# Performance work log

Measured on AMD Instinct MI355X. Metric: run time of the kernel, lower is better.

Reference implementation:

```python
import jax, jax.numpy as jnp
import numpy as np
import math

B, L, D = 4, 4096, 1024
PI = math.pi
LN_EPS = 1e-5


def setup_inputs() -> dict:
    key = jax.random.key(0)
    ks = jax.random.split(key, 16)
    s = 1.0 / math.sqrt(D)
    inp = {
        "x": jax.random.normal(ks[0], (B, L, D), dtype=jnp.float32),
        # Linear weights stored as [in, out] (torch W.T)
        "Wk": jax.random.normal(ks[1], (D, D), dtype=jnp.float32) * s,
        "bk": jnp.zeros((D,), dtype=jnp.float32),
        "Wq": jax.random.normal(ks[2], (D, D), dtype=jnp.float32) * s,
        "bq": jnp.zeros((D,), dtype=jnp.float32),
        "Wv": jax.random.normal(ks[3], (D, D), dtype=jnp.float32) * s,
        "bv": jnp.zeros((D,), dtype=jnp.float32),
        "ln_g": jnp.ones((D,), dtype=jnp.float32),
        "ln_b": jnp.zeros((D,), dtype=jnp.float32),
        "Wo": jax.random.normal(ks[4], (D, D), dtype=jnp.float32) * s,
        "bo": jnp.zeros((D,), dtype=jnp.float32),
        "Wg1": jax.random.normal(ks[5], (D, D // 4), dtype=jnp.float32) * s,
        "bg1": jnp.zeros((D // 4,), dtype=jnp.float32),
        "Wg2": jax.random.normal(ks[6], (D // 4, 1), dtype=jnp.float32) * (2.0 / math.sqrt(D)),
        "bg2": jnp.zeros((1,), dtype=jnp.float32),
        "pos_phases": jax.random.normal(ks[7], (L, D), dtype=jnp.float32) * PI,
    }
    return inp


def _layernorm(x, g, b):
    mu = jnp.mean(x, axis=-1, keepdims=True)
    var = jnp.var(x, axis=-1, keepdims=True)
    return (x - mu) * jax.lax.rsqrt(var + LN_EPS) * g + b


def reference(x, Wk, bk, Wq, bq, Wv, bv, ln_g, ln_b, Wo, bo, Wg1, bg1, Wg2, bg2, pos_phases):
    # dropout is identity in eval mode
    key_phases = jnp.tanh(x @ Wk + bk) * PI          # [B,L,D]
    query_phases = jnp.tanh(x @ Wq + bq) * PI        # [B,L,D]
    V = x @ Wv + bv                                   # [B,L,D]

    cos_k, sin_k = jnp.cos(key_phases), jnp.sin(key_phases)
    cos_q, sin_q = jnp.cos(query_phases), jnp.sin(query_phases)

    mem_real = jnp.cumsum(V * cos_k, axis=1)
    mem_imag = jnp.cumsum(V * sin_k, axis=1)
    content_retrieved = mem_real * cos_q + mem_imag * sin_q

    pp = pos_phases[: x.shape[1]]                     # [L,D]
    cos_p, sin_p = jnp.cos(pp), jnp.sin(pp)
    pos_mem_real = jnp.cumsum(V * cos_p, axis=1)
    pos_mem_imag = jnp.cumsum(V * sin_p, axis=1)
    pos_retrieved = pos_mem_real * cos_p + pos_mem_imag * sin_p

    gate = jax.nn.sigmoid(jax.nn.gelu(x @ Wg1 + bg1) @ Wg2 + bg2)  # [B,L,1]
    combined = gate * content_retrieved + (1.0 - gate) * pos_retrieved

    positions = jnp.arange(1, x.shape[1] + 1, dtype=jnp.float32)
    norm = jnp.sqrt(positions)[None, :, None]
    out = _layernorm(combined / norm, ln_g, ln_b) @ Wo + bo
    return x + out
```

## Files before the change

### kernel.cpp

```cpp
#include <hip/hip_runtime.h>
#include <math.h>

#define B_ 4
#define L_ 4096
#define D_ 1024
#define DG_ 256
#define NC_ 128
#define CL_ 32
#define PI_F 3.14159265358979323846f
#define LN_EPS_F 1e-5f

typedef __attribute__((ext_vector_type(8))) _Float16 f16x8;
typedef __attribute__((ext_vector_type(8))) short s16x8;
typedef __attribute__((ext_vector_type(4))) short s16x4;
typedef __attribute__((ext_vector_type(4))) float f32x4;

__device__ inline short f2h(float f) { return __builtin_bit_cast(short, (_Float16)f); }
__device__ inline float h2f(short s) { return (float)__builtin_bit_cast(_Float16, s); }

__device__ inline float ftanh(float x) {
    float e = __expf(2.0f * x);
    return 1.0f - 2.0f / (e + 1.0f);
}
__device__ inline void fsincos(float x, float* s, float* c) {
    *s = __sinf(x); *c = __cosf(x);
}

__device__ inline void gld16(const void* g, void* l) {
    __builtin_amdgcn_global_load_lds(
        (const __attribute__((address_space(1))) unsigned int*)g,
        (__attribute__((address_space(3))) unsigned int*)l, 16, 0, 0);
}

__global__ __launch_bounds__(256)
void conv_x(const float* __restrict__ x, short* __restrict__ xh, int n8)
{
    int t = blockIdx.x * 256 + threadIdx.x;
    if (t >= n8) return;
    const float4* p = (const float4*)x + (size_t)t * 2;
    float4 a = p[0], b = p[1];
    s16x8 v;
    v[0] = f2h(a.x); v[1] = f2h(a.y); v[2] = f2h(a.z); v[3] = f2h(a.w);
    v[4] = f2h(b.x); v[5] = f2h(b.y); v[6] = f2h(b.z); v[7] = f2h(b.w);
    *(s16x8*)(xh + (size_t)t * 8) = v;
}

__global__ __launch_bounds__(256)
void convT(const float* __restrict__ W, short* __restrict__ Th, int N)
{
    __shared__ float tile[64][65];
    const int n0 = blockIdx.x * 64, k0 = blockIdx.y * 64;
    const int t = threadIdx.x;
    const int r = t >> 4, c4 = (t & 15) * 4;

    #pragma unroll
    for (int i = 0; i < 4; ++i) {
        float4 v = *(const float4*)&W[(size_t)(k0 + r + i * 16) * N + n0 + c4];
        tile[r + i * 16][c4 + 0] = v.x;
        tile[r + i * 16][c4 + 1] = v.y;
        tile[r + i * 16][c4 + 2] = v.z;
        tile[r + i * 16][c4 + 3] = v.w;
    }
    __syncthreads();
    #pragma unroll
    for (int i = 0; i < 4; ++i) {
        const int n = r + i * 16;
        s16x4 o;
        o[0] = f2h(tile[c4 + 0][n]);
        o[1] = f2h(tile[c4 + 1][n]);
        o[2] = f2h(tile[c4 + 2][n]);
        o[3] = f2h(tile[c4 + 3][n]);
        *(s16x4*)&Th[(size_t)(n0 + n) * 1024 + k0 + c4] = o;
    }
}

#define BARRIER() __builtin_amdgcn_s_barrier()
#define PRIO1() __builtin_amdgcn_s_setprio(1)
#define PRIO0() __builtin_amdgcn_s_setprio(0)
#define LGKM0() do { asm volatile("s_waitcnt lgkmcnt(0)" ::: "memory"); \
                     __builtin_amdgcn_sched_barrier(0); } while (0)
#define VMC(N) asm volatile("s_waitcnt vmcnt(" #N ")" ::: "memory")

#define DSR(dst, areg, OFS)                                              \
    asm volatile("ds_read_b128 %0, %1 offset:" OFS                       \
                 : "=v"(dst) : "v"(areg))

#define RDA4(areg)                                                       \
    DSR(af[0], areg, "0");    DSR(af[1], areg, "2048");                  \
    DSR(af[2], areg, "4096"); DSR(af[3], areg, "6144");
#define RDA4H(areg)                                                      \
    DSR(af[0], areg, "8192");  DSR(af[1], areg, "10240");                \
    DSR(af[2], areg, "12288"); DSR(af[3], areg, "14336");
#define RDB4(areg, KK)                                                   \
    DSR(bq[0][KK], areg, "0");    DSR(bq[1][KK], areg, "2048");          \
    DSR(bq[2][KK], areg, "4096"); DSR(bq[3][KK], areg, "6144");

#define MF(MG, KK)                                                       \
    _Pragma("unroll") for (int i_ = 0; i_ < 4; ++i_)                     \
    _Pragma("unroll") for (int n_ = 0; n_ < 4; ++n_)                     \
        acc[(MG)*4 + i_][n_] = __builtin_amdgcn_mfma_f32_16x16x32_f16(   \
            af[i_], bq[n_][KK], acc[(MG)*4 + i_][n_], 0, 0, 0);

template<int EPI, typename OT>
__global__ __launch_bounds__(512, 2)
void mgemm256(const short* __restrict__ A, const short* __restrict__ Bt,
              const float* __restrict__ X, OT* __restrict__ out0,
              short* __restrict__ out1, short* __restrict__ out2,
              const float* __restrict__ b0, const float* __restrict__ b1,
              const float* __restrict__ b2, int M, int N, int K)
{
    extern __shared__ char lds[];

    const int tid = threadIdx.x;
    const int w = tid >> 6, l = tid & 63;
    const int wr = w >> 2, wc = w & 3;
    const int fr = l & 15, kb = l >> 4;
    const int bm = blockIdx.x * 256, bn = blockIdx.y * 256;
    const int np = K >> 7;

    const int s = fr & 7;
    const int cK0 = (((s >> 2) & 1) << 6) | (((kb ^ s) & 3) << 4);
    const int aA0 = (wr << 14) + fr * 128 + cK0;
    const int aA1 = aA0 ^ 64;
    const int aB0 = 32768 + ((wc >> 1) << 14) + ((wc & 1) * 64 + fr) * 128 + cK0;
    const int aB1 = aB0 ^ 64;
    const int aA0o = aA0 + 65536, aA1o = aA1 + 65536;
    const int aB0o = aB0 + 65536, aB1o = aB1 + 65536;

    const int p0 = tid * 16;
    const int sr = p0 >> 7;
    const int sc = (p0 & 127) ^ ((sr & 7) << 4);
    const short* gA = A  + (size_t)(bm + sr) * K + (sc >> 1);
    const short* gB = Bt + (size_t)(bn + sr) * K + (sc >> 1);
    char* ldst = lds + (w << 10);
    const size_t q1 = (size_t)64 * K, q2 = 2 * q1, q3 = 3 * q1;

    f32x4 acc[8][4] = {};
    f16x8 af[4];
    f16x8 bq[4][2];

    gld16(gA,      ldst);          gld16(gA + q1, ldst + 8192);
    gld16(gA + q2, ldst + 16384);  gld16(gA + q3, ldst + 24576);
    gld16(gB,      ldst + 32768);  gld16(gB + q1, ldst + 40960);
    gld16(gB + q2, ldst + 49152);  gld16(gB + q3, ldst + 57344);
    gld16(gA +      64, ldst + 65536);
    gld16(gA + q2 + 64, ldst + 65536 + 16384);
    VMC(2);
    BARRIER();

    const short* gAn = gA + 64;
    const short* gBn = gB + 64;

    for (int pp = 0; pp < np; ++pp) {
        const bool nl = (pp + 1 < np);

        RDA4(aA0); RDB4(aB0, 0);
        gld16(gBn,      ldst + 98304);
        gld16(gBn + q1, ldst + 98304 + 8192);
        BARRIER();
        LGKM0();
        PRIO1(); MF(0, 0); PRIO0();
        BARRIER();

        RDA4(aA1); RDB4(aB1, 1);
        gld16(gBn + q2, ldst + 98304 + 16384);
        gld16(gBn + q3, ldst + 98304 + 24576);
        BARRIER();
        LGKM0();
        PRIO1(); MF(0, 1); PRIO0();
        BARRIER();

        RDA4H(aA0);
        gld16(gAn + q1, ldst + 65536 + 8192);
        gld16(gAn + q3, ldst + 65536 + 24576);
        BARRIER();
        LGKM0();
        PRIO1(); MF(1, 0); PRIO0();
        BARRIER();

        RDA4H(aA1);
        if (nl) { gld16(gAn + 64, ldst); gld16(gAn + 64 + q2, ldst + 16384); }
        BARRIER();
        LGKM0();
        PRIO1(); MF(1, 1); PRIO0();
        VMC(2);
        BARRIER();

        RDA4(aA0o); RDB4(aB0o, 0);
        if (nl) {
            gld16(gBn +      64, ldst + 32768);
            gld16(gBn + q1 + 64, ldst + 40960);
        }
        BARRIER();
        LGKM0();
        PRIO1(); MF(0, 0); PRIO0();
        BARRIER();

        RDA4(aA1o); RDB4(aB1o, 1);
        if (nl) {
            gld16(gBn + q2 + 64, ldst + 49152);
            gld16(gBn + q3 + 64, ldst + 57344);
        }
        BARRIER();
        LGKM0();
        PRIO1(); MF(0, 1); PRIO0();
        BARRIER();

        if (!nl) VMC(0);
        RDA4H(aA0o);
        if (nl) {
            gld16(gAn + q1 + 64, ldst + 8192);
            gld16(gAn + q3 + 64, ldst + 24576);
        }
        BARRIER();
        LGKM0();
        PRIO1(); MF(1, 0); PRIO0();
        BARRIER();

        RDA4H(aA1o);
        if (nl) { gld16(gAn + 128, ldst + 65536); gld16(gAn + 128 + q2, ldst + 65536 + 16384); }
        BARRIER();
        LGKM0();
        PRIO1(); MF(1, 1); PRIO0();
        if (nl) {
            VMC(2);
            BARRIER();
        }
        gAn += 128; gBn += 128;
    }

    if constexpr (EPI == 4) {
        short* op; const float* bp; bool dt;
        if (bn < 1024)      { op = (short*)out0; bp = b0; dt = true;  }
        else if (bn < 2048) { op = out1;         bp = b1; dt = true;  }
        else                { op = out2;         bp = b2; dt = false; }
        const int cb = bn & 1023;
        float bc[4];
        #pragma unroll
        for (int nf = 0; nf < 4; ++nf) bc[nf] = bp[cb + wc * 64 + nf * 16 + fr];
        #pragma unroll
        for (int mf = 0; mf < 8; ++mf)
            #pragma unroll
            for (int rr = 0; rr < 4; ++rr) {
                const int row = bm + wr * 128 + mf * 16 + kb * 4 + rr;
                #pragma unroll
                for (int nf = 0; nf < 4; ++nf) {
                    const int cc = cb + wc * 64 + nf * 16 + fr;
                    float c = acc[mf][nf][rr] + bc[nf];
                    if (dt) c = ftanh(c) * PI_F;
                    op[(size_t)row * 1024 + cc] = f2h(c);
                }
            }
    } else {
        float bc[4];
        #pragma unroll
        for (int nf = 0; nf < 4; ++nf) bc[nf] = b0[bn + wc * 64 + nf * 16 + fr];
        #pragma unroll
        for (int mf = 0; mf < 8; ++mf)
            #pragma unroll
            for (int rr = 0; rr < 4; ++rr) {
                const int row = bm + wr * 128 + mf * 16 + kb * 4 + rr;
                #pragma unroll
                for (int nf = 0; nf < 4; ++nf) {
                    const int col = bn + wc * 64 + nf * 16 + fr;
                    float c = acc[mf][nf][rr] + bc[nf] + X[(size_t)row * N + col];
                    ((float*)out0)[(size_t)row * N + col] = c;
                }
            }
    }
}

#define RDAF(areg)                                                       \
    DSR(af[0], areg, "0");    DSR(af[1], areg, "2048");                  \
    DSR(af[2], areg, "4096"); DSR(af[3], areg, "6144");
#define RDBF(areg)                                                       \
    DSR(bqs[0], areg, "0");    DSR(bqs[1], areg, "2048");                \
    DSR(bqs[2], areg, "4096"); DSR(bqs[3], areg, "6144");

#define MF16()                                                           \
    _Pragma("unroll") for (int i_ = 0; i_ < 4; ++i_)                     \
    _Pragma("unroll") for (int n_ = 0; n_ < 4; ++n_)                     \
        acc[i_][n_] = __builtin_amdgcn_mfma_f32_16x16x32_f16(            \
            af[i_], bqs[n_], acc[i_][n_], 0, 0, 0);

template<int EPI>
__global__ __launch_bounds__(256, 2)
void gemm128(const short* __restrict__ A, const short* __restrict__ Bt,
             const float* __restrict__ b0, const float* __restrict__ wg2p,
             float* __restrict__ gatep, int M, int N, int K)
{
    extern __shared__ char lds[];

    const int tid = threadIdx.x;
    const int w = tid >> 6, l = tid & 63;
    const int wr = w >> 1, wc = w & 1;
    const int fr = l & 15, kb = l >> 4;
    const int bm = blockIdx.x * 128, bn = blockIdx.y * 128;

    const int s = fr & 7;
    const int cK0 = (((s >> 2) & 1) << 6) | (((kb ^ s) & 3) << 4);
    const int aA0e = (wr * 64 + fr) * 128 + cK0;
    const int aA1e = aA0e ^ 64;
    const int aB0e = 16384 + (wc * 64 + fr) * 128 + cK0;
    const int aB1e = aB0e ^ 64;
    const int aA0o = aA0e + 32768, aA1o = aA1e + 32768;
    const int aB0o = aB0e + 32768, aB1o = aB1e + 32768;

    const int p16 = tid * 16;
    const int sr = p16 >> 7;
    const int sc = (p16 & 127) ^ ((sr & 7) << 4);
    const short* gA = A  + (size_t)(bm + sr) * K + (sc >> 1);
    const short* gB = Bt + (size_t)(bn + sr) * K + (sc >> 1);
    char* ldA = lds + (w << 10);
    const size_t r32 = (size_t)32 * K;

    f32x4 acc[4][4] = {};
    f16x8 af[4], bqs[4];

    #pragma unroll
    for (int i = 0; i < 4; ++i) gld16(gA + i * r32, ldA + i * 4096);
    #pragma unroll
    for (int i = 0; i < 4; ++i) gld16(gB + i * r32, ldA + 16384 + i * 4096);
    VMC(0);
    BARRIER();

    const short* gAt = gA;
    const short* gBt = gB;
    const int np = K >> 7;

    for (int pp = 0; pp < np; ++pp) {
        const bool nl = (pp + 1 < np);

        RDAF(aA0e); RDBF(aB0e);
        #pragma unroll
        for (int i = 0; i < 4; ++i) gld16(gAt + 64 + i * r32, ldA + 32768 + i * 4096);
        LGKM0();
        PRIO1(); MF16(); PRIO0();
        RDAF(aA1e); RDBF(aB1e);
        #pragma unroll
        for (int i = 0; i < 4; ++i) gld16(gBt + 64 + i * r32, ldA + 49152 + i * 4096);
        LGKM0();
        PRIO1(); MF16(); PRIO0();
        VMC(0);
        BARRIER();

        RDAF(aA0o); RDBF(aB0o);
        if (nl) {
            #pragma unroll
            for (int i = 0; i < 4; ++i) gld16(gAt + 128 + i * r32, ldA + i * 4096);
        }
        LGKM0();
        PRIO1(); MF16(); PRIO0();
        RDAF(aA1o); RDBF(aB1o);
        if (nl) {
            #pragma unroll
            for (int i = 0; i < 4; ++i) gld16(gBt + 128 + i * r32, ldA + 16384 + i * 4096);
        }
        LGKM0();
        PRIO1(); MF16(); PRIO0();
        if (nl) {
            VMC(0);
            BARRIER();
        }
        gAt += 128; gBt += 128;
    }

    float bg[4], wg[4];
    #pragma unroll
    for (int nf = 0; nf < 4; ++nf) {
        const int cl = bn + wc * 64 + nf * 16 + fr;
        bg[nf] = b0[cl];
        wg[nf] = wg2p[cl];
    }
    #pragma unroll
    for (int mf = 0; mf < 4; ++mf)
        #pragma unroll
        for (int rr = 0; rr < 4; ++rr) {
            const int row = bm + wr * 64 + mf * 16 + kb * 4 + rr;
            float part = 0.f;
            #pragma unroll
            for (int nf = 0; nf < 4; ++nf) {
                float c = acc[mf][nf][rr] + bg[nf];
                float tt = 0.7978845608028654f * (c + 0.044715f * c * c * c);
                float g = 0.5f * c * (1.0f + ftanh(tt));
                part += g * wg[nf];
            }
            part += __shfl_xor(part, 1);
            part += __shfl_xor(part, 2);
            part += __shfl_xor(part, 4);
            part += __shfl_xor(part, 8);
            if (fr == 0) atomicAdd(&gatep[row], part);
        }
}

__global__ __launch_bounds__(256)
void passA(const short* __restrict__ V, const short* __restrict__ KP,
           const float* __restrict__ PP, f32x4* __restrict__ SI)
{
    const int bid = blockIdx.x;
    const int b = bid >> 7, c = bid & 127;
    const int d0 = threadIdx.x * 4;

    f32x4 cr = {}, ci = {}, pr = {}, pi = {};
    const size_t base  = ((size_t)b * L_ + (size_t)c * CL_) * D_ + d0;
    const size_t pbase = (size_t)c * CL_ * D_ + d0;
    for (int ll = 0; ll < CL_; ++ll) {
        s16x4 v4  = *(const s16x4*)&V [base + (size_t)ll * D_];
        s16x4 kp4 = *(const s16x4*)&KP[base + (size_t)ll * D_];
        f32x4 pp4 = *(const f32x4*)&PP[pbase + (size_t)ll * D_];
        #pragma unroll
        for (int j = 0; j < 4; ++j) {
            float v = h2f(v4[j]);
            float sk, ck, sp, cp;
            fsincos(h2f(kp4[j]), &sk, &ck);
            fsincos(pp4[j], &sp, &cp);
            cr[j] += v * ck; ci[j] += v * sk;
            pr[j] += v * cp; pi[j] += v * sp;
        }
    }
    const size_t sidx = ((size_t)bid << 10) + d0;
    #pragma unroll
    for (int j = 0; j < 4; ++j) {
        f32x4 o = { cr[j], ci[j], pr[j], pi[j] };
        SI[sidx + j] = o;
    }
}

__global__ __launch_bounds__(256)
void passB(f32x4* __restrict__ SI)
{
    const int t = blockIdx.x * 256 + threadIdx.x;
    const int b = t >> 10, d = t & 1023;
    f32x4 run = {};
    for (int c = 0; c < NC_; ++c) {
        const size_t idx = ((size_t)(b * NC_ + c) << 10) + d;
        f32x4 v = SI[idx];
        SI[idx] = run;
        run += v;
    }
}

__global__ __launch_bounds__(256)
void passC(const short* __restrict__ V, const short* KP,
           const short* __restrict__ QP, const float* __restrict__ PP,
           const float* __restrict__ gatep, const float* __restrict__ bg2,
           const f32x4* __restrict__ SI, const float* __restrict__ ln_g,
           const float* __restrict__ ln_b, short* Yb)
{
    const int bid = blockIdx.x;
    const int b = bid >> 7, c = bid & 127;
    const int d0 = threadIdx.x * 4;

    const size_t sidx = ((size_t)bid << 10) + d0;
    f32x4 cr, ci, pr, pi;
    #pragma unroll
    for (int j = 0; j < 4; ++j) {
        f32x4 s = SI[sidx + j];
        cr[j] = s[0]; ci[j] = s[1]; pr[j] = s[2]; pi[j] = s[3];
    }
    const f32x4 g_ln = *(const f32x4*)&ln_g[d0];
    const f32x4 b_ln = *(const f32x4*)&ln_b[d0];
    const float bg2v = bg2[0];

    __shared__ float2 lred[2][4];
    const int wid = threadIdx.x >> 6;
    const int lane = threadIdx.x & 63;

    for (int l0 = 0; l0 < CL_; ++l0) {
        const int ll = c * CL_ + l0;
        const size_t off = ((size_t)b * L_ + ll) * D_ + d0;
        s16x4 v4  = *(const s16x4*)&V [off];
        s16x4 kp4 = *(const s16x4*)&KP[off];
        s16x4 qp4 = *(const s16x4*)&QP[off];
        f32x4 pp4 = *(const f32x4*)&PP[(size_t)ll * D_ + d0];
        const float gv = 1.0f / (1.0f + __expf(-(gatep[b * L_ + ll] + bg2v)));
        const float rs_pos = rsqrtf((float)(ll + 1));

        f32x4 u;
        #pragma unroll
        for (int j = 0; j < 4; ++j) {
            float v = h2f(v4[j]);
            float sk, ck, sq, cq, sp, cp;
            fsincos(h2f(kp4[j]), &sk, &ck);
            fsincos(h2f(qp4[j]), &sq, &cq);
            fsincos(pp4[j], &sp, &cp);
            cr[j] += v * ck; ci[j] += v * sk;
            pr[j] += v * cp; pi[j] += v * sp;
            float content = cr[j] * cq + ci[j] * sq;
            float posr    = pr[j] * cp + pi[j] * sp;
            u[j] = (gv * content + (1.0f - gv) * posr) * rs_pos;
        }

        float s  = u[0] + u[1] + u[2] + u[3];
        float s2 = u[0]*u[0] + u[1]*u[1] + u[2]*u[2] + u[3]*u[3];
        #pragma unroll
        for (int o = 32; o; o >>= 1) {
            s  += __shfl_down(s, o);
            s2 += __shfl_down(s2, o);
        }
        const int pb = l0 & 1;
        if (lane == 0) lred[pb][wid] = make_float2(s, s2);
        __syncthreads();
        float ts  = lred[pb][0].x + lred[pb][1].x + lred[pb][2].x + lred[pb][3].x;
        float ts2 = lred[pb][0].y + lred[pb][1].y + lred[pb][2].y + lred[pb][3].y;
        const float mu  = ts * (1.0f / D_);
        const float var = ts2 * (1.0f / D_) - mu * mu;
        const float rsv = rsqrtf(var + LN_EPS_F);
        s16x4 yo;
        #pragma unroll
        for (int j = 0; j < 4; ++j)
            yo[j] = f2h((u[j] - mu) * rsv * g_ln[j] + b_ln[j]);
        *(s16x4*)&Yb[off] = yo;
    }
}

extern "C" void kernel_launch(void* const* d_in, const int* in_sizes, int n_in,
                              void* d_out, int out_size, void* d_ws, size_t ws_size,
                              hipStream_t stream)
{
    const float* x    = (const float*)d_in[0];
    const float* Wk   = (const float*)d_in[1];
    const float* bk   = (const float*)d_in[2];
    const float* Wq   = (const float*)d_in[3];
    const float* bq   = (const float*)d_in[4];
    const float* Wv   = (const float*)d_in[5];
    const float* bv   = (const float*)d_in[6];
    const float* ln_g = (const float*)d_in[7];
    const float* ln_b = (const float*)d_in[8];
    const float* Wo   = (const float*)d_in[9];
    const float* bo   = (const float*)d_in[10];
    const float* Wg1  = (const float*)d_in[11];
    const float* bg1  = (const float*)d_in[12];
    const float* Wg2  = (const float*)d_in[13];
    const float* bg2  = (const float*)d_in[14];
    const float* PP   = (const float*)d_in[15];

    float* out = (float*)d_out;

    const size_t BLD   = (size_t)B_ * L_ * D_;
    const size_t SZ_X  = BLD * 2;
    const size_t SZ_R1 = (size_t)B_ * L_ * DG_ * 2;
    const size_t SZ_G1 = (size_t)D_ * DG_ * 2;
    const size_t SZ_GT = (size_t)B_ * L_ * 4;
    const size_t NEED  = SZ_X + SZ_R1 + SZ_G1 + 3 * SZ_X + SZ_GT;
    if (ws_size < NEED) {
        hipMemcpyAsync(d_out, d_in[0], BLD * sizeof(float),
                       hipMemcpyDeviceToDevice, stream);
        return;
    }

    char* wsb = (char*)d_ws;
    short* xh   = (short*)(wsb);
    char*  r1   = wsb + SZ_X;
    short* Wcat = (short*)r1;
    short* Wg1T = (short*)(r1 + SZ_R1);
    short* KP   = (short*)(r1 + SZ_R1 + SZ_G1);
    short* QP   = (short*)((char*)KP + SZ_X);
    short* V    = (short*)((char*)QP + SZ_X);
    float* gatep = (float*)((char*)V + SZ_X);
    short* WtO  = (short*)(wsb);
    f32x4* SI   = (f32x4*)(wsb + 2097152);
    short* Yb   = KP;

    const int M = B_ * L_;
    dim3 blk(256);

    conv_x<<<(int)(BLD / 8 / 256), blk, 0, stream>>>(x, xh, (int)(BLD / 8));
    dim3 gT(D_ / 64, 16);
    dim3 gTg(DG_ / 64, 16);
    convT<<<gT, blk, 0, stream>>>(Wk, Wcat + (size_t)0 * D_ * D_, D_);
    convT<<<gT, blk, 0, stream>>>(Wq, Wcat + (size_t)1 * D_ * D_, D_);
    convT<<<gT, blk, 0, stream>>>(Wv, Wcat + (size_t)2 * D_ * D_, D_);
    convT<<<gTg, blk, 0, stream>>>(Wg1, Wg1T, DG_);
    hipMemsetAsync(gatep, 0, SZ_GT, stream);

    dim3 gQKV(M / 256, 3072 / 256);
    hipLaunchKernelGGL((mgemm256<4, short>), gQKV, dim3(512), 131072, stream,
                       xh, Wcat, nullptr, KP, QP, V, bk, bq, bv, M, 3072, D_);
    dim3 gH(M / 128, DG_ / 128);
    hipLaunchKernelGGL((gemm128<5>), gH, blk, 65536, stream,
                       xh, Wg1T, bg1, Wg2, gatep, M, DG_, D_);

    convT<<<gT, blk, 0, stream>>>(Wo, WtO, D_);

    passA<<<B_ * NC_, blk, 0, stream>>>(V, KP, PP, SI);
    passB<<<(B_ * D_) / 256, blk, 0, stream>>>(SI);
    passC<<<B_ * NC_, blk, 0, stream>>>(V, KP, QP, PP, gatep, bg2, SI,
                                        ln_g, ln_b, Yb);

    dim3 gO(M / 256, D_ / 256);
    hipLaunchKernelGGL((mgemm256<3, float>), gO, dim3(512), 131072, stream,
                       Yb, WtO, x, out, nullptr, nullptr, bo, nullptr, nullptr,
                       M, D_, D_);
}
```

Baseline: 291.5 us.

## Halve scan chunk length, drop GEMM barriers, prefetch rows in passC

Three changes land together. The scan chunk length goes from 32 to 16, so passA/passC launch twice as many blocks for more parallelism, at the cost of a longer serial prefix pass. The GEMM main loop drops most of its paired barriers around each MFMA sub-step and keeps one barrier per half-iteration, which cuts sync overhead but risks LDS races if the buffers overlap. passC now software-prefetches the next row's V/KP/QP/PP/gate values and swaps __syncthreads for a raw lgkmcnt wait plus s_barrier.

```diff
diff --git a/kernel.cpp b/kernel.cpp
--- a/kernel.cpp
+++ b/kernel.cpp
@@ -5,8 +5,8 @@
 #define L_ 4096
 #define D_ 1024
 #define DG_ 256
-#define NC_ 128
-#define CL_ 32
+#define NC_ 256
+#define CL_ 16
 #define PI_F 3.14159265358979323846f
 #define LN_EPS_F 1e-5f
 
@@ -157,33 +157,24 @@
         RDA4(aA0); RDB4(aB0, 0);
         gld16(gBn,      ldst + 98304);
         gld16(gBn + q1, ldst + 98304 + 8192);
-        BARRIER();
         LGKM0();
         PRIO1(); MF(0, 0); PRIO0();
-        BARRIER();
-
         RDA4(aA1); RDB4(aB1, 1);
         gld16(gBn + q2, ldst + 98304 + 16384);
         gld16(gBn + q3, ldst + 98304 + 24576);
-        BARRIER();
         LGKM0();
         PRIO1(); MF(0, 1); PRIO0();
         BARRIER();
-
         RDA4H(aA0);
         gld16(gAn + q1, ldst + 65536 + 8192);
         gld16(gAn + q3, ldst + 65536 + 24576);
-        BARRIER();
         LGKM0();
         PRIO1(); MF(1, 0); PRIO0();
-        BARRIER();
-
         RDA4H(aA1);
         if (nl) { gld16(gAn + 64, ldst); gld16(gAn + 64 + q2, ldst + 16384); }
-        BARRIER();
         LGKM0();
         PRIO1(); MF(1, 1); PRIO0();
-        VMC(2);
+        if (nl) { VMC(2); } else { VMC(0); }
         BARRIER();
 
         RDA4(aA0o); RDB4(aB0o, 0);
@@ -191,35 +182,25 @@
             gld16(gBn +      64, ldst + 32768);
             gld16(gBn + q1 + 64, ldst + 40960);
         }
-        BARRIER();
         LGKM0();
         PRIO1(); MF(0, 0); PRIO0();
-        BARRIER();
-
         RDA4(aA1o); RDB4(aB1o, 1);
         if (nl) {
             gld16(gBn + q2 + 64, ldst + 49152);
             gld16(gBn + q3 + 64, ldst + 57344);
         }
-        BARRIER();
         LGKM0();
         PRIO1(); MF(0, 1); PRIO0();
         BARRIER();
-
-        if (!nl) VMC(0);
         RDA4H(aA0o);
         if (nl) {
             gld16(gAn + q1 + 64, ldst + 8192);
             gld16(gAn + q3 + 64, ldst + 24576);
         }
-        BARRIER();
         LGKM0();
         PRIO1(); MF(1, 0); PRIO0();
-        BARRIER();
-
         RDA4H(aA1o);
         if (nl) { gld16(gAn + 128, ldst + 65536); gld16(gAn + 128 + q2, ldst + 65536 + 16384); }
-        BARRIER();
         LGKM0();
         PRIO1(); MF(1, 1); PRIO0();
         if (nl) {
@@ -398,7 +379,7 @@
            const float* __restrict__ PP, f32x4* __restrict__ SI)
 {
     const int bid = blockIdx.x;
-    const int b = bid >> 7, c = bid & 127;
+    const int b = bid >> 8, c = bid & 255;
     const int d0 = threadIdx.x * 4;
 
     f32x4 cr = {}, ci = {}, pr = {}, pi = {};
@@ -448,15 +429,15 @@
            const float* __restrict__ ln_b, short* Yb)
 {
     const int bid = blockIdx.x;
-    const int b = bid >> 7, c = bid & 127;
+    const int b = bid >> 8, c = bid & 255;
     const int d0 = threadIdx.x * 4;
 
     const size_t sidx = ((size_t)bid << 10) + d0;
     f32x4 cr, ci, pr, pi;
     #pragma unroll
     for (int j = 0; j < 4; ++j) {
-        f32x4 s = SI[sidx + j];
-        cr[j] = s[0]; ci[j] = s[1]; pr[j] = s[2]; pi[j] = s[3];
+        f32x4 s0 = SI[sidx + j];
+        cr[j] = s0[0]; ci[j] = s0[1]; pr[j] = s0[2]; pi[j] = s0[3];
     }
     const f32x4 g_ln = *(const f32x4*)&ln_g[d0];
     const f32x4 b_ln = *(const f32x4*)&ln_b[d0];
@@ -466,14 +447,28 @@
     const int wid = threadIdx.x >> 6;
     const int lane = threadIdx.x & 63;
 
+    const int lbase = c * CL_;
+    size_t off = ((size_t)b * L_ + lbase) * D_ + d0;
+    s16x4 v4  = *(const s16x4*)&V [off];
+    s16x4 kp4 = *(const s16x4*)&KP[off];
+    s16x4 qp4 = *(const s16x4*)&QP[off];
+    f32x4 pp4 = *(const f32x4*)&PP[(size_t)lbase * D_ + d0];
+    float gpre = gatep[b * L_ + lbase];
+
     for (int l0 = 0; l0 < CL_; ++l0) {
-        const int ll = c * CL_ + l0;
-        const size_t off = ((size_t)b * L_ + ll) * D_ + d0;
-        s16x4 v4  = *(const s16x4*)&V [off];
-        s16x4 kp4 = *(const s16x4*)&KP[off];
-        s16x4 qp4 = *(const s16x4*)&QP[off];
-        f32x4 pp4 = *(const f32x4*)&PP[(size_t)ll * D_ + d0];
-        const float gv = 1.0f / (1.0f + __expf(-(gatep[b * L_ + ll] + bg2v)));
+        const int ll = lbase + l0;
+        const size_t offn = off + D_;
+        s16x4 v4n = v4, kp4n = kp4, qp4n = qp4;
+        f32x4 pp4n = pp4; float gpn = gpre;
+        if (l0 + 1 < CL_) {
+            v4n  = *(const s16x4*)&V [offn];
+            kp4n = *(const s16x4*)&KP[offn];
+            qp4n = *(const s16x4*)&QP[offn];
+            pp4n = *(const f32x4*)&PP[(size_t)(ll + 1) * D_ + d0];
+            gpn  = gatep[b * L_ + ll + 1];
+        }
+
+        const float gv = 1.0f / (1.0f + __expf(-(gpre + bg2v)));
         const float rs_pos = rsqrtf((float)(ll + 1));
 
         f32x4 u;
@@ -500,7 +495,8 @@
         }
         const int pb = l0 & 1;
         if (lane == 0) lred[pb][wid] = make_float2(s, s2);
-        __syncthreads();
+        asm volatile("s_waitcnt lgkmcnt(0)" ::: "memory");
+        __builtin_amdgcn_s_barrier();
         float ts  = lred[pb][0].x + lred[pb][1].x + lred[pb][2].x + lred[pb][3].x;
         float ts2 = lred[pb][0].y + lred[pb][1].y + lred[pb][2].y + lred[pb][3].y;
         const float mu  = ts * (1.0f / D_);
@@ -511,6 +507,9 @@
         for (int j = 0; j < 4; ++j)
             yo[j] = f2h((u[j] - mu) * rsv * g_ln[j] + b_ln[j]);
         *(s16x4*)&Yb[off] = yo;
+
+        off = offn;
+        v4 = v4n; kp4 = kp4n; qp4 = qp4n; pp4 = pp4n; gpre = gpn;
     }
 }
 
```

After: 290.6 us. No clear change (-0.3%).
